# Kernel tuning notes

Measured on AMD Instinct MI355X. Metric: run time of the kernel, lower is better.

Reference implementation:

```python
import jax, jax.numpy as jnp
import numpy as np
import math

IN_DIM = 3
WIDTH = 256
DEPTH = 6
OUT_DIM = 1
W0_FIRST = 30.0
W0_HIDDEN = 1.0
N_POINTS = 1048576


def _uniform(key, shape, bound):
    return jax.random.uniform(key, shape, dtype=jnp.float32, minval=-bound, maxval=bound)


def setup_inputs() -> dict:
    key = jax.random.key(0)
    ks = jax.random.split(key, 8)
    xyt = jax.random.uniform(ks[0], (N_POINTS, IN_DIM), dtype=jnp.float32, minval=-1.0, maxval=1.0)
    # first layer: bound = 1/in_features
    W0 = _uniform(ks[1], (WIDTH, IN_DIM), 1.0 / IN_DIM)
    b0 = jnp.zeros((WIDTH,), jnp.float32)
    # hidden layers: bound = sqrt(6/width)/w0_hidden
    hb = math.sqrt(6.0 / WIDTH) / W0_HIDDEN
    W1 = _uniform(ks[2], (WIDTH, WIDTH), hb)
    b1 = jnp.zeros((WIDTH,), jnp.float32)
    W2 = _uniform(ks[3], (WIDTH, WIDTH), hb)
    b2 = jnp.zeros((WIDTH,), jnp.float32)
    W3 = _uniform(ks[4], (WIDTH, WIDTH), hb)
    b3 = jnp.zeros((WIDTH,), jnp.float32)
    W4 = _uniform(ks[5], (WIDTH, WIDTH), hb)
    b4 = jnp.zeros((WIDTH,), jnp.float32)
    Wf = _uniform(ks[6], (OUT_DIM, WIDTH), hb)
    bf = jnp.zeros((OUT_DIM,), jnp.float32)
    return {"xyt": xyt, "W0": W0, "b0": b0, "W1": W1, "b1": b1,
            "W2": W2, "b2": b2, "W3": W3, "b3": b3, "W4": W4, "b4": b4,
            "Wf": Wf, "bf": bf}


def reference(xyt, W0, b0, W1, b1, W2, b2, W3, b3, W4, b4, Wf, bf):
    # SineLayer: sin(w0 * (x @ W^T + b)); torch Linear weight is [out, in]
    h = jnp.sin(W0_FIRST * (xyt @ W0.T + b0))          # [N, 256]
    for W, b in ((W1, b1), (W2, b2), (W3, b3), (W4, b4)):
        h = jnp.sin(W0_HIDDEN * (h @ W.T + b))          # [N, 256]
    out = h @ Wf.T + bf                                  # [N, 1]
    return out.squeeze(-1)                               # [N]
```

## Files before the change

kernel.cpp:

```cpp
#include <hip/hip_runtime.h>

typedef _Float16 half8 __attribute__((ext_vector_type(8)));
typedef _Float16 half4 __attribute__((ext_vector_type(4)));
typedef float f32x4 __attribute__((ext_vector_type(4)));

#define WPAD 264
#define NPB 128
#define THREADS 512
#define INV2PI 0.15915494309189535f
#define W0SCALE (30.0f * INV2PI)
#define SMEM_BYTES (NPB * WPAD * 2 + (384 + 256) * 4)

__global__ void convert_weights(const float* __restrict__ W1, const float* __restrict__ W2,
                                const float* __restrict__ W3, const float* __restrict__ W4,
                                _Float16* __restrict__ Wc) {
    int tid = blockIdx.x * 256 + threadIdx.x;
    int l   = tid >> 16;
    int rem = tid & 65535;
    int n = rem >> 8, k = rem & 255;
    const float* W = (l == 0) ? W1 : (l == 1) ? W2 : (l == 2) ? W3 : W4;
    int kc = k >> 5, kl = k & 31;
    Wc[l * 65536 + kc * 8192 + n * 32 + kl] = (_Float16)(W[rem] * INV2PI);
}

__launch_bounds__(THREADS, 4)
__global__ void siren_fused(const float* __restrict__ xyt,
                            const float* __restrict__ W0,
                            const float* __restrict__ b0,
                            const _Float16* __restrict__ Wc,
                            const float* __restrict__ b1,
                            const float* __restrict__ b2,
                            const float* __restrict__ b3,
                            const float* __restrict__ b4,
                            const float* __restrict__ Wf,
                            const float* __restrict__ bfin,
                            float* __restrict__ out)
{
    extern __shared__ _Float16 smem[];
    _Float16* hbuf = smem;
    float* xs   = (float*)(smem + NPB * WPAD);
    float* wf_s = xs + 384;

    const int tid  = threadIdx.x;
    const int lane = tid & 63;
    const int wv   = tid >> 6;
    const int l15  = lane & 15;
    const int l4   = lane >> 4;
    const int gm0  = blockIdx.x * NPB;

    if (tid < 384) xs[tid] = xyt[gm0 * 3 + tid];
    if (tid < 256) wf_s[tid] = Wf[tid];
    __syncthreads();

    {
        const int fg = lane;
        const int p0 = wv * 16;
        float w[4][3], bb[4];
        #pragma unroll
        for (int c = 0; c < 4; ++c) {
            const int n = fg * 4 + c;
            w[c][0] = W0[n * 3 + 0] * W0SCALE;
            w[c][1] = W0[n * 3 + 1] * W0SCALE;
            w[c][2] = W0[n * 3 + 2] * W0SCALE;
            bb[c]   = b0[n] * W0SCALE;
        }
        #pragma unroll 4
        for (int p = 0; p < 16; ++p) {
            const float x0 = xs[(p0 + p) * 3], x1 = xs[(p0 + p) * 3 + 1], x2 = xs[(p0 + p) * 3 + 2];
            half4 hv;
            #pragma unroll
            for (int c = 0; c < 4; ++c) {
                float z = fmaf(w[c][0], x0, fmaf(w[c][1], x1, fmaf(w[c][2], x2, bb[c])));
                hv[c] = (_Float16)__builtin_amdgcn_sinf(z);
            }
            *(half4*)&hbuf[(p0 + p) * WPAD + fg * 4] = hv;
        }
    }

    const int arow = (wv * 32 + l15) * 32 + l4 * 8;

    #pragma unroll
    for (int l = 0; l < 4; ++l) {
        const float* bl = (l == 0) ? b1 : (l == 1) ? b2 : (l == 2) ? b3 : b4;
        const _Float16* wl = Wc + l * 65536;

        half8 areg[2][2];
        #pragma unroll
        for (int c = 0; c < 2; ++c)
            #pragma unroll
            for (int i = 0; i < 2; ++i)
                areg[c][i] = *(const half8*)&wl[c * 8192 + arow + i * 512];

        f32x4 acc[2][8];
        #pragma unroll
        for (int i = 0; i < 2; ++i) {
            f32x4 bb = *(const f32x4*)&bl[wv * 32 + i * 16 + l4 * 4];
            bb *= INV2PI;
            #pragma unroll
            for (int j = 0; j < 8; ++j)
                acc[i][j] = bb;
        }

        __syncthreads();

        #pragma unroll
        for (int kc = 0; kc < 8; ++kc) {
            half8 anext[2];
            if (kc < 6) {
                #pragma unroll
                for (int i = 0; i < 2; ++i)
                    anext[i] = *(const half8*)&wl[(kc + 2) * 8192 + arow + i * 512];
            }
            #pragma unroll
            for (int g = 0; g < 2; ++g) {
                half8 bfr[4];
                #pragma unroll
                for (int j = 0; j < 4; ++j)
                    bfr[j] = *(const half8*)&hbuf[((g * 4 + j) * 16 + l15) * WPAD + kc * 32 + l4 * 8];
                #pragma unroll
                for (int i = 0; i < 2; ++i)
                    #pragma unroll
                    for (int j = 0; j < 4; ++j)
                        acc[i][g * 4 + j] = __builtin_amdgcn_mfma_f32_16x16x32_f16(
                            areg[kc & 1][i], bfr[j], acc[i][g * 4 + j], 0, 0, 0);
            }
            if (kc < 6) { areg[kc & 1][0] = anext[0]; areg[kc & 1][1] = anext[1]; }
        }

        __syncthreads();

        #pragma unroll
        for (int i = 0; i < 2; ++i)
            #pragma unroll
            for (int j = 0; j < 8; ++j) {
                half4 hv;
                #pragma unroll
                for (int r = 0; r < 4; ++r)
                    hv[r] = (_Float16)__builtin_amdgcn_sinf(acc[i][j][r]);
                *(half4*)&hbuf[(j * 16 + l15) * WPAD + wv * 32 + i * 16 + l4 * 4] = hv;
            }
    }

    __syncthreads();

    {
        const int m = tid >> 2, q = tid & 3;
        const _Float16* hrow = &hbuf[m * WPAD + q * 64];
        float sum = 0.f;
        #pragma unroll
        for (int i = 0; i < 8; ++i) {
            half8 hv = *(const half8*)&hrow[i * 8];
            const int nb = q * 64 + i * 8;
            #pragma unroll
            for (int j = 0; j < 8; ++j)
                sum = fmaf((float)hv[j], wf_s[nb + j], sum);
        }
        sum += __shfl_down(sum, 2);
        sum += __shfl_down(sum, 1);
        if (q == 0) out[gm0 + m] = sum + bfin[0];
    }
}

extern "C" void kernel_launch(void* const* d_in, const int* in_sizes, int n_in,
                              void* d_out, int out_size, void* d_ws, size_t ws_size,
                              hipStream_t stream) {
    const float* xyt = (const float*)d_in[0];
    const float* W0  = (const float*)d_in[1];
    const float* b0  = (const float*)d_in[2];
    const float* W1  = (const float*)d_in[3];
    const float* b1  = (const float*)d_in[4];
    const float* W2  = (const float*)d_in[5];
    const float* b2  = (const float*)d_in[6];
    const float* W3  = (const float*)d_in[7];
    const float* b3  = (const float*)d_in[8];
    const float* W4  = (const float*)d_in[9];
    const float* b4  = (const float*)d_in[10];
    const float* Wf  = (const float*)d_in[11];
    const float* bf  = (const float*)d_in[12];
    float* out = (float*)d_out;
    _Float16* Wc = (_Float16*)d_ws;

    hipFuncSetAttribute((const void*)siren_fused,
                        hipFuncAttributeMaxDynamicSharedMemorySize, SMEM_BYTES);

    convert_weights<<<1024, 256, 0, stream>>>(W1, W2, W3, W4, Wc);

    const int N = in_sizes[0] / 3;
    siren_fused<<<N / NPB, THREADS, SMEM_BYTES, stream>>>(
        xyt, W0, b0, Wc, b1, b2, b3, b4, Wf, bf, out);
}
```

Baseline: 598.9 us.

## Shrink point tile to 96 and raise occupancy with fewer accumulators

Reduces points per block from 128 to 96, which cuts accumulator registers and LDS per block, and raises the launch-bounds occupancy hint from 4 to 6. The double-buffered weight-fragment prefetch is replaced by direct per-chunk loads, MFMA sections are wrapped in s_setprio, and the sine evaluation moves ahead of the barrier so it overlaps with other waves. A tail guard handles N not divisible by 96. The trade-off is less weight reuse per block and exposed global-load latency, in exchange for more resident waves.

```diff
diff --git a/kernel.cpp b/kernel.cpp
--- a/kernel.cpp
+++ b/kernel.cpp
@@ -5,11 +5,11 @@
 typedef float f32x4 __attribute__((ext_vector_type(4)));
 
 #define WPAD 264
-#define NPB 128
+#define NPB 96
 #define THREADS 512
 #define INV2PI 0.15915494309189535f
 #define W0SCALE (30.0f * INV2PI)
-#define SMEM_BYTES (NPB * WPAD * 2 + (384 + 256) * 4)
+#define SMEM_BYTES (NPB * WPAD * 2 + (288 + 256) * 4)
 
 __global__ void convert_weights(const float* __restrict__ W1, const float* __restrict__ W2,
                                 const float* __restrict__ W3, const float* __restrict__ W4,
@@ -23,7 +23,7 @@
     Wc[l * 65536 + kc * 8192 + n * 32 + kl] = (_Float16)(W[rem] * INV2PI);
 }
 
-__launch_bounds__(THREADS, 4)
+__launch_bounds__(THREADS, 6)
 __global__ void siren_fused(const float* __restrict__ xyt,
                             const float* __restrict__ W0,
                             const float* __restrict__ b0,
@@ -34,12 +34,13 @@
                             const float* __restrict__ b4,
                             const float* __restrict__ Wf,
                             const float* __restrict__ bfin,
-                            float* __restrict__ out)
+                            float* __restrict__ out,
+                            int npts)
 {
     extern __shared__ _Float16 smem[];
     _Float16* hbuf = smem;
     float* xs   = (float*)(smem + NPB * WPAD);
-    float* wf_s = xs + 384;
+    float* wf_s = xs + 288;
 
     const int tid  = threadIdx.x;
     const int lane = tid & 63;
@@ -47,14 +48,15 @@
     const int l15  = lane & 15;
     const int l4   = lane >> 4;
     const int gm0  = blockIdx.x * NPB;
+    const int nv   = min(NPB, npts - gm0);
 
-    if (tid < 384) xs[tid] = xyt[gm0 * 3 + tid];
+    if (tid < nv * 3) xs[tid] = xyt[gm0 * 3 + tid];
     if (tid < 256) wf_s[tid] = Wf[tid];
     __syncthreads();
 
     {
         const int fg = lane;
-        const int p0 = wv * 16;
+        const int p0 = wv * 12;
         float w[4][3], bb[4];
         #pragma unroll
         for (int c = 0; c < 4; ++c) {
@@ -65,7 +67,7 @@
             bb[c]   = b0[n] * W0SCALE;
         }
         #pragma unroll 4
-        for (int p = 0; p < 16; ++p) {
+        for (int p = 0; p < 12; ++p) {
             const float x0 = xs[(p0 + p) * 3], x1 = xs[(p0 + p) * 3 + 1], x2 = xs[(p0 + p) * 3 + 2];
             half4 hv;
             #pragma unroll
@@ -84,20 +86,13 @@
         const float* bl = (l == 0) ? b1 : (l == 1) ? b2 : (l == 2) ? b3 : b4;
         const _Float16* wl = Wc + l * 65536;
 
-        half8 areg[2][2];
-        #pragma unroll
-        for (int c = 0; c < 2; ++c)
-            #pragma unroll
-            for (int i = 0; i < 2; ++i)
-                areg[c][i] = *(const half8*)&wl[c * 8192 + arow + i * 512];
-
-        f32x4 acc[2][8];
+        f32x4 acc[2][6];
         #pragma unroll
         for (int i = 0; i < 2; ++i) {
             f32x4 bb = *(const f32x4*)&bl[wv * 32 + i * 16 + l4 * 4];
             bb *= INV2PI;
             #pragma unroll
-            for (int j = 0; j < 8; ++j)
+            for (int j = 0; j < 6; ++j)
                 acc[i][j] = bb;
         }
 
@@ -105,59 +100,63 @@
 
         #pragma unroll
         for (int kc = 0; kc < 8; ++kc) {
-            half8 anext[2];
-            if (kc < 6) {
-                #pragma unroll
-                for (int i = 0; i < 2; ++i)
-                    anext[i] = *(const half8*)&wl[(kc + 2) * 8192 + arow + i * 512];
-            }
+            half8 a0 = *(const half8*)&wl[kc * 8192 + arow];
+            half8 a1 = *(const half8*)&wl[kc * 8192 + arow + 512];
             #pragma unroll
             for (int g = 0; g < 2; ++g) {
-                half8 bfr[4];
+                half8 bfr[3];
                 #pragma unroll
-                for (int j = 0; j < 4; ++j)
-                    bfr[j] = *(const half8*)&hbuf[((g * 4 + j) * 16 + l15) * WPAD + kc * 32 + l4 * 8];
+                for (int j = 0; j < 3; ++j)
+                    bfr[j] = *(const half8*)&hbuf[((g * 3 + j) * 16 + l15) * WPAD + kc * 32 + l4 * 8];
+                __builtin_amdgcn_s_setprio(1);
                 #pragma unroll
-                for (int i = 0; i < 2; ++i)
-                    #pragma unroll
-                    for (int j = 0; j < 4; ++j)
-                        acc[i][g * 4 + j] = __builtin_amdgcn_mfma_f32_16x16x32_f16(
-                            areg[kc & 1][i], bfr[j], acc[i][g * 4 + j], 0, 0, 0);
+                for (int j = 0; j < 3; ++j) {
+                    acc[0][g * 3 + j] = __builtin_amdgcn_mfma_f32_16x16x32_f16(
+                        a0, bfr[j], acc[0][g * 3 + j], 0, 0, 0);
+                    acc[1][g * 3 + j] = __builtin_amdgcn_mfma_f32_16x16x32_f16(
+                        a1, bfr[j], acc[1][g * 3 + j], 0, 0, 0);
+                }
+                __builtin_amdgcn_s_setprio(0);
             }
-            if (kc < 6) { areg[kc & 1][0] = anext[0]; areg[kc & 1][1] = anext[1]; }
         }
+
+        half4 hv[2][6];
+        #pragma unroll
+        for (int i = 0; i < 2; ++i)
+            #pragma unroll
+            for (int j = 0; j < 6; ++j)
+                #pragma unroll
+                for (int r = 0; r < 4; ++r)
+                    hv[i][j][r] = (_Float16)__builtin_amdgcn_sinf(acc[i][j][r]);
 
         __syncthreads();
 
         #pragma unroll
         for (int i = 0; i < 2; ++i)
             #pragma unroll
-            for (int j = 0; j < 8; ++j) {
-                half4 hv;
-                #pragma unroll
-                for (int r = 0; r < 4; ++r)
-                    hv[r] = (_Float16)__builtin_amdgcn_sinf(acc[i][j][r]);
-                *(half4*)&hbuf[(j * 16 + l15) * WPAD + wv * 32 + i * 16 + l4 * 4] = hv;
-            }
+            for (int j = 0; j < 6; ++j)
+                *(half4*)&hbuf[(j * 16 + l15) * WPAD + wv * 32 + i * 16 + l4 * 4] = hv[i][j];
     }
 
     __syncthreads();
 
     {
         const int m = tid >> 2, q = tid & 3;
-        const _Float16* hrow = &hbuf[m * WPAD + q * 64];
-        float sum = 0.f;
-        #pragma unroll
-        for (int i = 0; i < 8; ++i) {
-            half8 hv = *(const half8*)&hrow[i * 8];
-            const int nb = q * 64 + i * 8;
+        if (m < nv) {
+            const _Float16* hrow = &hbuf[m * WPAD + q * 64];
+            float sum = 0.f;
             #pragma unroll
-            for (int j = 0; j < 8; ++j)
-                sum = fmaf((float)hv[j], wf_s[nb + j], sum);
+            for (int i = 0; i < 8; ++i) {
+                half8 hv = *(const half8*)&hrow[i * 8];
+                const int nb = q * 64 + i * 8;
+                #pragma unroll
+                for (int j = 0; j < 8; ++j)
+                    sum = fmaf((float)hv[j], wf_s[nb + j], sum);
+            }
+            sum += __shfl_down(sum, 2);
+            sum += __shfl_down(sum, 1);
+            if (q == 0) out[gm0 + m] = sum + bfin[0];
         }
-        sum += __shfl_down(sum, 2);
-        sum += __shfl_down(sum, 1);
-        if (q == 0) out[gm0 + m] = sum + bfin[0];
     }
 }
 
@@ -186,6 +185,7 @@
     convert_weights<<<1024, 256, 0, stream>>>(W1, W2, W3, W4, Wc);
 
     const int N = in_sizes[0] / 3;
-    siren_fused<<<N / NPB, THREADS, SMEM_BYTES, stream>>>(
-        xyt, W0, b0, Wc, b1, b2, b3, b4, Wf, bf, out);
+    const int grid = (N + NPB - 1) / NPB;
+    siren_fused<<<grid, THREADS, SMEM_BYTES, stream>>>(
+        xyt, W0, b0, Wc, b1, b2, b3, b4, Wf, bf, out, N);
 }
```

New measurement: 653.7 us. 9.1% more time.
